# Optimization experiments

Measured on AMD Instinct MI355X. Metric: run time of the kernel, lower is better.

Reference implementation:

```python
import jax, jax.numpy as jnp
import numpy as np

N_SAMPLES = 128
NUM_OBJECTS = 8
NUM_POINTS = 100000


def setup_inputs() -> dict:
    key = jax.random.key(0)
    k = jax.random.split(key, 7)
    obj_id = jax.random.randint(k[0], (N_SAMPLES,), 0, NUM_OBJECTS)
    gt_cam_R_m2c = jax.random.normal(k[1], (N_SAMPLES, 3, 3), dtype=jnp.float32)
    pred_cam_R_m2c = jax.random.normal(k[2], (N_SAMPLES, 3, 3), dtype=jnp.float32)
    gt_cam_t_m2c_site = jax.random.normal(k[3], (N_SAMPLES, 3), dtype=jnp.float32)
    pred_cam_t_m2c_site = jax.random.normal(k[4], (N_SAMPLES, 3), dtype=jnp.float32)
    obj_points = jax.random.normal(k[5], (NUM_OBJECTS, NUM_POINTS, 3), dtype=jnp.float32)
    # diameters strictly positive (we divide by them)
    obj_diameters = jax.random.uniform(k[6], (NUM_OBJECTS,), dtype=jnp.float32) + 0.5
    return {
        'obj_id': obj_id,
        'gt_cam_R_m2c': gt_cam_R_m2c,
        'pred_cam_R_m2c': pred_cam_R_m2c,
        'gt_cam_t_m2c_site': gt_cam_t_m2c_site,
        'pred_cam_t_m2c_site': pred_cam_t_m2c_site,
        'obj_points': obj_points,
        'obj_diameters': obj_diameters,
    }


def reference(obj_id, gt_cam_R_m2c, pred_cam_R_m2c, gt_cam_t_m2c_site,
              pred_cam_t_m2c_site, obj_points, obj_diameters):
    # --- pm_loss: ADD metric with p=1, divided by object diameter ---
    # per-sample mesh points: [N, P, 3]
    pts = obj_points[obj_id]
    # rotation difference applied to every mesh point: [N, P, 3]
    dR = pred_cam_R_m2c - gt_cam_R_m2c            # [N, 3, 3]
    moved = jnp.einsum('nij,npj->npi', dR, pts)   # [N, P, 3]
    # L1 norm per point, mean over points -> [N]
    pm = jnp.abs(moved).sum(axis=-1).mean(axis=-1)
    pm = pm / obj_diameters[obj_id]

    # --- t_site_center_loss: L1 norm over xy -> [N] ---
    t_center = jnp.abs(gt_cam_t_m2c_site[:, :2] - pred_cam_t_m2c_site[:, :2]).sum(axis=-1)

    # --- t_site_depth_loss: abs diff of z -> [N] ---
    t_depth = jnp.abs(gt_cam_t_m2c_site[:, 2] - pred_cam_t_m2c_site[:, 2])

    return pm, t_center, t_depth
```

## Files before the change

kernel.cpp:

```cpp
#include <hip/hip_runtime.h>

#define N_SAMPLES 128
#define NUM_OBJECTS 8
#define NUM_POINTS 100000
#define GROUPS 25000
#define TPB 256
#define CHUNKS 98
#define MAXS 128

__device__ __forceinline__ float pts4_l1(
    const float* __restrict__ f,
    float d0, float d1, float d2, float d3, float d4,
    float d5, float d6, float d7, float d8)
{
    float s;
    s  = fabsf(d0 * f[0] + d1 * f[1]  + d2 * f[2])
       + fabsf(d3 * f[0] + d4 * f[1]  + d5 * f[2])
       + fabsf(d6 * f[0] + d7 * f[1]  + d8 * f[2]);
    s += fabsf(d0 * f[3] + d1 * f[4]  + d2 * f[5])
       + fabsf(d3 * f[3] + d4 * f[4]  + d5 * f[5])
       + fabsf(d6 * f[3] + d7 * f[4]  + d8 * f[5]);
    s += fabsf(d0 * f[6] + d1 * f[7]  + d2 * f[8])
       + fabsf(d3 * f[6] + d4 * f[7]  + d5 * f[8])
       + fabsf(d6 * f[6] + d7 * f[7]  + d8 * f[8]);
    s += fabsf(d0 * f[9] + d1 * f[10] + d2 * f[11])
       + fabsf(d3 * f[9] + d4 * f[10] + d5 * f[11])
       + fabsf(d6 * f[9] + d7 * f[10] + d8 * f[11]);
    return s;
}

__global__ __launch_bounds__(TPB) void pm_partial_kernel(
    const int* __restrict__ obj_id,
    const float* __restrict__ gtR, const float* __restrict__ prR,
    const float* __restrict__ pts,
    float* __restrict__ ws)
{
    const int o     = blockIdx.y;
    const int chunk = blockIdx.x;

    __shared__ int   s_cnt;
    __shared__ int   s_sidx[MAXS];
    __shared__ float s_dR[MAXS][12];
    __shared__ float s_part[8][MAXS];

    if (threadIdx.x == 0) s_cnt = 0;
    __syncthreads();
    if (threadIdx.x < N_SAMPLES) {
        const int n = threadIdx.x;
        if (obj_id[n] == o) {
            int slot = atomicAdd(&s_cnt, 1);
            s_sidx[slot] = n;
            #pragma unroll
            for (int j = 0; j < 9; ++j)
                s_dR[slot][j] = prR[n * 9 + j] - gtR[n * 9 + j];
        }
    }
    __syncthreads();
    const int nsamp = s_cnt;
    if (nsamp == 0) return;
    const int nsamp_pad = (nsamp + 3) & ~3;
    {
        const int idx = nsamp + (int)threadIdx.x;
        if (idx < nsamp_pad) {
            #pragma unroll
            for (int j = 0; j < 9; ++j) s_dR[idx][j] = 0.0f;
        }
    }
    __syncthreads();

    int g = chunk * TPB + threadIdx.x;
    const float valid = (g < GROUPS) ? 1.0f : 0.0f;
    g = min(g, GROUPS - 1);
    const float4* __restrict__ p4 =
        (const float4*)(pts + (size_t)o * (size_t)NUM_POINTS * 3);
    float4 a = p4[g * 3 + 0];
    float4 b = p4[g * 3 + 1];
    float4 c = p4[g * 3 + 2];
    float f[12] = { a.x * valid, a.y * valid, a.z * valid, a.w * valid,
                    b.x * valid, b.y * valid, b.z * valid, b.w * valid,
                    c.x * valid, c.y * valid, c.z * valid, c.w * valid };

    const int lane = threadIdx.x & 63;
    const int wave = threadIdx.x >> 6;
    const int half = wave * 2 + (lane >> 5);

    for (int s0 = 0; s0 < nsamp_pad; s0 += 4) {
        float acc[4];
        #pragma unroll
        for (int k = 0; k < 4; ++k) {
            float4 q0 = *(const float4*)&s_dR[s0 + k][0];
            float4 q1 = *(const float4*)&s_dR[s0 + k][4];
            float4 q2 = *(const float4*)&s_dR[s0 + k][8];
            acc[k] = pts4_l1(f, q0.x, q0.y, q0.z, q0.w,
                                q1.x, q1.y, q1.z, q1.w, q2.x);
        }
        #pragma unroll
        for (int off = 1; off <= 16; off <<= 1) {
            #pragma unroll
            for (int k = 0; k < 4; ++k)
                acc[k] += __shfl_xor(acc[k], off, 64);
        }
        if ((lane & 31) == 0) {
            #pragma unroll
            for (int k = 0; k < 4; ++k)
                s_part[half][s0 + k] = acc[k];
        }
    }
    __syncthreads();

    if (threadIdx.x < nsamp) {
        const int s = threadIdx.x;
        float v = 0.0f;
        #pragma unroll
        for (int w = 0; w < 8; ++w) v += s_part[w][s];
        ws[(size_t)s_sidx[s] * CHUNKS + chunk] = v;
    }
}

__global__ __launch_bounds__(64) void finish_kernel(
    const int* __restrict__ obj_id, const float* __restrict__ diam,
    const float* __restrict__ gt_t, const float* __restrict__ pred_t,
    const float* __restrict__ ws, float* __restrict__ out)
{
    const int n = blockIdx.x;
    const int t = threadIdx.x;

    float v = ws[(size_t)n * CHUNKS + t];
    if (t + 64 < CHUNKS) v += ws[(size_t)n * CHUNKS + t + 64];

    #pragma unroll
    for (int off = 32; off > 0; off >>= 1)
        v += __shfl_down(v, off, 64);

    if (t == 0) {
        out[n] = v / ((float)NUM_POINTS * diam[obj_id[n]]);
    } else if (t == 1) {
        out[N_SAMPLES + n] = fabsf(gt_t[n * 3 + 0] - pred_t[n * 3 + 0])
                           + fabsf(gt_t[n * 3 + 1] - pred_t[n * 3 + 1]);
    } else if (t == 2) {
        out[2 * N_SAMPLES + n] = fabsf(gt_t[n * 3 + 2] - pred_t[n * 3 + 2]);
    }
}

extern "C" void kernel_launch(void* const* d_in, const int* in_sizes, int n_in,
                              void* d_out, int out_size, void* d_ws, size_t ws_size,
                              hipStream_t stream) {
    const int*   obj_id = (const int*)d_in[0];
    const float* gtR    = (const float*)d_in[1];
    const float* prR    = (const float*)d_in[2];
    const float* gt_t   = (const float*)d_in[3];
    const float* pred_t = (const float*)d_in[4];
    const float* pts    = (const float*)d_in[5];
    const float* diam   = (const float*)d_in[6];
    float* out = (float*)d_out;
    float* ws  = (float*)d_ws;

    pm_partial_kernel<<<dim3(CHUNKS, NUM_OBJECTS), TPB, 0, stream>>>(
        obj_id, gtR, prR, pts, ws);
    finish_kernel<<<N_SAMPLES, 64, 0, stream>>>(
        obj_id, diam, gt_t, pred_t, ws, out);
}
```

Before: 17.37 us.

## Precompute per-object rotation deltas in prep kernel and process two point groups per thread

Adds a single-block prep kernel that buckets samples by object, writes padded rotation deltas and sample indices to workspace, and computes the translation losses. The main kernel then loads the deltas from workspace instead of redoing the per-block scan and atomics. Each thread now handles two groups of four points, with the chunk count reduced from 98 to 64. The intent is to amortise the per-sample shared-memory loop over more points per thread, at the cost of an extra kernel launch and fewer blocks.

```diff
diff --git a/kernel.cpp b/kernel.cpp
--- a/kernel.cpp
+++ b/kernel.cpp
@@ -5,8 +5,13 @@
 #define NUM_POINTS 100000
 #define GROUPS 25000
 #define TPB 256
-#define CHUNKS 98
+#define CHUNKS 64
 #define MAXS 128
+
+#define WS_PART 0
+#define WS_CNT  8192
+#define WS_SIDX 8200
+#define WS_DR   9224
 
 __device__ __forceinline__ float pts4_l1(
     const float* __restrict__ f,
@@ -29,60 +34,74 @@
     return s;
 }
 
-__global__ __launch_bounds__(TPB) void pm_partial_kernel(
+__global__ __launch_bounds__(256) void prep_kernel(
     const int* __restrict__ obj_id,
     const float* __restrict__ gtR, const float* __restrict__ prR,
-    const float* __restrict__ pts,
-    float* __restrict__ ws)
+    const float* __restrict__ gt_t, const float* __restrict__ pred_t,
+    float* __restrict__ ws, float* __restrict__ out)
+{
+    __shared__ int s_cnt[NUM_OBJECTS];
+    const int t = threadIdx.x;
+    if (t < NUM_OBJECTS) s_cnt[t] = 0;
+    __syncthreads();
+    if (t < N_SAMPLES) {
+        const int n = t;
+        const int o = obj_id[n];
+        const int slot = atomicAdd(&s_cnt[o], 1);
+        ((int*)(ws + WS_SIDX))[o * MAXS + slot] = n;
+        float* dr = ws + WS_DR + ((size_t)o * MAXS + slot) * 12;
+        #pragma unroll
+        for (int j = 0; j < 9; ++j)
+            dr[j] = prR[n * 9 + j] - gtR[n * 9 + j];
+        dr[9] = 0.0f; dr[10] = 0.0f; dr[11] = 0.0f;
+        out[N_SAMPLES + n] = fabsf(gt_t[n * 3 + 0] - pred_t[n * 3 + 0])
+                           + fabsf(gt_t[n * 3 + 1] - pred_t[n * 3 + 1]);
+        out[2 * N_SAMPLES + n] = fabsf(gt_t[n * 3 + 2] - pred_t[n * 3 + 2]);
+    }
+    __syncthreads();
+    if (t < NUM_OBJECTS) ((int*)(ws + WS_CNT))[t] = s_cnt[t];
+}
+
+__global__ __launch_bounds__(TPB) void pm_partial_kernel(
+    const float* __restrict__ pts, float* __restrict__ ws)
 {
     const int o     = blockIdx.y;
     const int chunk = blockIdx.x;
+    const int tid   = threadIdx.x;
 
-    __shared__ int   s_cnt;
+    const int nsamp = ((const int*)(ws + WS_CNT))[o];
+    if (nsamp == 0) return;
+    const int nsamp_pad = (nsamp + 3) & ~3;
+
+    __shared__ float s_dR[MAXS][12];
     __shared__ int   s_sidx[MAXS];
-    __shared__ float s_dR[MAXS][12];
     __shared__ float s_part[8][MAXS];
 
-    if (threadIdx.x == 0) s_cnt = 0;
-    __syncthreads();
-    if (threadIdx.x < N_SAMPLES) {
-        const int n = threadIdx.x;
-        if (obj_id[n] == o) {
-            int slot = atomicAdd(&s_cnt, 1);
-            s_sidx[slot] = n;
-            #pragma unroll
-            for (int j = 0; j < 9; ++j)
-                s_dR[slot][j] = prR[n * 9 + j] - gtR[n * 9 + j];
-        }
-    }
-    __syncthreads();
-    const int nsamp = s_cnt;
-    if (nsamp == 0) return;
-    const int nsamp_pad = (nsamp + 3) & ~3;
-    {
-        const int idx = nsamp + (int)threadIdx.x;
-        if (idx < nsamp_pad) {
-            #pragma unroll
-            for (int j = 0; j < 9; ++j) s_dR[idx][j] = 0.0f;
-        }
-    }
+    const float4* __restrict__ dR4 =
+        (const float4*)(ws + WS_DR + (size_t)o * MAXS * 12);
+    float4* s_dR4 = (float4*)&s_dR[0][0];
+    for (int i = tid; i < nsamp_pad * 3; i += TPB)
+        s_dR4[i] = (i < nsamp * 3) ? dR4[i] : make_float4(0.f, 0.f, 0.f, 0.f);
+    const int* __restrict__ sidx = (const int*)(ws + WS_SIDX) + o * MAXS;
+    if (tid < nsamp) s_sidx[tid] = sidx[tid];
     __syncthreads();
 
-    int g = chunk * TPB + threadIdx.x;
-    const float valid = (g < GROUPS) ? 1.0f : 0.0f;
-    g = min(g, GROUPS - 1);
     const float4* __restrict__ p4 =
         (const float4*)(pts + (size_t)o * (size_t)NUM_POINTS * 3);
-    float4 a = p4[g * 3 + 0];
-    float4 b = p4[g * 3 + 1];
-    float4 c = p4[g * 3 + 2];
-    float f[12] = { a.x * valid, a.y * valid, a.z * valid, a.w * valid,
-                    b.x * valid, b.y * valid, b.z * valid, b.w * valid,
-                    c.x * valid, c.y * valid, c.z * valid, c.w * valid };
+    const int g0 = chunk * TPB + tid;
+    const int g1 = g0 + CHUNKS * TPB;
+    float4 a0 = p4[g0 * 3 + 0], b0 = p4[g0 * 3 + 1], c0 = p4[g0 * 3 + 2];
+    const float valid = (g1 < GROUPS) ? 1.0f : 0.0f;
+    const int g1c = min(g1, GROUPS - 1);
+    float4 a1 = p4[g1c * 3 + 0], b1 = p4[g1c * 3 + 1], c1 = p4[g1c * 3 + 2];
+    float f0[12] = { a0.x, a0.y, a0.z, a0.w, b0.x, b0.y,
+                     b0.z, b0.w, c0.x, c0.y, c0.z, c0.w };
+    float f1[12] = { a1.x * valid, a1.y * valid, a1.z * valid, a1.w * valid,
+                     b1.x * valid, b1.y * valid, b1.z * valid, b1.w * valid,
+                     c1.x * valid, c1.y * valid, c1.z * valid, c1.w * valid };
 
-    const int lane = threadIdx.x & 63;
-    const int wave = threadIdx.x >> 6;
-    const int half = wave * 2 + (lane >> 5);
+    const int lane = tid & 63;
+    const int half = (tid >> 6) * 2 + ((lane >> 5) & 1);
 
     for (int s0 = 0; s0 < nsamp_pad; s0 += 4) {
         float acc[4];
@@ -91,8 +110,10 @@
             float4 q0 = *(const float4*)&s_dR[s0 + k][0];
             float4 q1 = *(const float4*)&s_dR[s0 + k][4];
             float4 q2 = *(const float4*)&s_dR[s0 + k][8];
-            acc[k] = pts4_l1(f, q0.x, q0.y, q0.z, q0.w,
-                                q1.x, q1.y, q1.z, q1.w, q2.x);
+            acc[k] = pts4_l1(f0, q0.x, q0.y, q0.z, q0.w,
+                                 q1.x, q1.y, q1.z, q1.w, q2.x)
+                   + pts4_l1(f1, q0.x, q0.y, q0.z, q0.w,
+                                 q1.x, q1.y, q1.z, q1.w, q2.x);
         }
         #pragma unroll
         for (int off = 1; off <= 16; off <<= 1) {
@@ -108,38 +129,26 @@
     }
     __syncthreads();
 
-    if (threadIdx.x < nsamp) {
-        const int s = threadIdx.x;
+    if (tid < nsamp) {
         float v = 0.0f;
         #pragma unroll
-        for (int w = 0; w < 8; ++w) v += s_part[w][s];
-        ws[(size_t)s_sidx[s] * CHUNKS + chunk] = v;
+        for (int w = 0; w < 8; ++w) v += s_part[w][tid];
+        ws[WS_PART + (size_t)s_sidx[tid] * CHUNKS + chunk] = v;
     }
 }
 
 __global__ __launch_bounds__(64) void finish_kernel(
     const int* __restrict__ obj_id, const float* __restrict__ diam,
-    const float* __restrict__ gt_t, const float* __restrict__ pred_t,
     const float* __restrict__ ws, float* __restrict__ out)
 {
     const int n = blockIdx.x;
     const int t = threadIdx.x;
-
-    float v = ws[(size_t)n * CHUNKS + t];
-    if (t + 64 < CHUNKS) v += ws[(size_t)n * CHUNKS + t + 64];
-
+    float v = ws[WS_PART + (size_t)n * CHUNKS + t];
     #pragma unroll
-    for (int off = 32; off > 0; off >>= 1)
-        v += __shfl_down(v, off, 64);
-
-    if (t == 0) {
+    for (int off = 1; off <= 32; off <<= 1)
+        v += __shfl_xor(v, off, 64);
+    if (t == 0)
         out[n] = v / ((float)NUM_POINTS * diam[obj_id[n]]);
-    } else if (t == 1) {
-        out[N_SAMPLES + n] = fabsf(gt_t[n * 3 + 0] - pred_t[n * 3 + 0])
-                           + fabsf(gt_t[n * 3 + 1] - pred_t[n * 3 + 1]);
-    } else if (t == 2) {
-        out[2 * N_SAMPLES + n] = fabsf(gt_t[n * 3 + 2] - pred_t[n * 3 + 2]);
-    }
 }
 
 extern "C" void kernel_launch(void* const* d_in, const int* in_sizes, int n_in,
@@ -155,8 +164,7 @@
     float* out = (float*)d_out;
     float* ws  = (float*)d_ws;
 
-    pm_partial_kernel<<<dim3(CHUNKS, NUM_OBJECTS), TPB, 0, stream>>>(
-        obj_id, gtR, prR, pts, ws);
-    finish_kernel<<<N_SAMPLES, 64, 0, stream>>>(
-        obj_id, diam, gt_t, pred_t, ws, out);
+    prep_kernel<<<1, 256, 0, stream>>>(obj_id, gtR, prR, gt_t, pred_t, ws, out);
+    pm_partial_kernel<<<dim3(CHUNKS, NUM_OBJECTS), TPB, 0, stream>>>(pts, ws);
+    finish_kernel<<<N_SAMPLES, 64, 0, stream>>>(obj_id, diam, ws, out);
 }
```

New measurement: 22.46 us. +29.3%, slower.
